# Kernel optimization log

Measured on AMD Instinct MI355X. Metric: run time of the kernel, lower is better.

## Reference

```python
import jax, jax.numpy as jnp
import numpy as np

B, S, K, D = 128, 64, 10, 256
THR = -1.5


def setup_inputs() -> dict:
    key = jax.random.key(0)
    ks = jax.random.split(key, 9)
    si = 1.0 / np.sqrt(D)  # torch GRU init: U(-1/sqrt(hidden), 1/sqrt(hidden))
    u = lambda k, shape, s: jax.random.uniform(k, shape, jnp.float32, -s, s)
    return {
        "item_embs": jax.random.normal(ks[0], (B, S, K, D), jnp.float32),
        "user_embs": jax.random.normal(ks[1], (B, S, D), jnp.float32),
        "W_ih": u(ks[2], (3 * D, 2 * D), si),
        "W_hh": u(ks[3], (3 * D, D), si),
        "b_ih": u(ks[4], (3 * D,), si),
        "b_hh": u(ks[5], (3 * D,), si),
        "w_out": u(ks[6], (D,), si),
        "b_out": u(ks[7], (), si),
        "length": jax.random.randint(ks[8], (B,), 0, S),
    }


def reference(item_embs, user_embs, W_ih, W_hh, b_ih, b_hh, w_out, b_out, length):
    N = B * S
    # x['items'] = cat([item_embs.flatten(0,1), zeros_like(...)], -1)  -> [N, K, 2D]
    items_flat = item_embs.reshape(N, K, D)
    items = jnp.concatenate([items_flat, jnp.zeros_like(items_flat)], axis=-1)
    # user hidden state: gather user_embs at (length-1, clamped), repeat over S
    idx = jnp.clip(length - 1, 0, None)  # [B]
    u0 = user_embs[jnp.arange(B), idx]   # [B, D]
    h0 = jnp.repeat(u0, S, axis=0)       # [N, D]

    def gru_cell(x, h):
        gi = x @ W_ih.T + b_ih  # [N, 3D]
        gh = h @ W_hh.T + b_hh
        i_r, i_z, i_n = jnp.split(gi, 3, axis=-1)
        h_r, h_z, h_n = jnp.split(gh, 3, axis=-1)
        r = jax.nn.sigmoid(i_r + h_r)
        z = jax.nn.sigmoid(i_z + h_z)
        n = jnp.tanh(i_n + r * h_n)
        return (1.0 - z) * n + z * h

    def step(carry, x_t):
        h, mask = carry  # mask [N,1]: readout threshold gate for the click-half of input
        x = jnp.concatenate([x_t[:, :D], x_t[:, D:] * mask], axis=-1)
        h = gru_cell(x, h)
        y = h @ w_out + b_out  # [N]
        next_mask = (jax.lax.stop_gradient(y) > THR).astype(x_t.dtype)[:, None]
        return (h, next_mask), y

    xs = jnp.swapaxes(items, 0, 1)  # [K, N, 2D]
    init = (h0, jnp.ones((N, 1), item_embs.dtype))
    _, ys = jax.lax.scan(step, init, xs)  # ys [K, N]
    y = jnp.swapaxes(ys, 0, 1)  # [N, K]
    # self.w = 1, self.b = 0 -> identity calibration
    return y.reshape(B, S, K)
```

## Files before the change

### kernel.cpp

```cpp
#include <hip/hip_runtime.h>

#define BB 128
#define SS 64
#define KK 10
#define DD 256
#define NN (BB*SS)
#define ROWS 32
#define NBLK (NN/ROWS)
#define NT 1024

typedef __attribute__((ext_vector_type(8))) short short8;
typedef __attribute__((ext_vector_type(4))) float f32x4;

#define FRAG_ELEMS (48*8*64*8)

__device__ __forceinline__ unsigned short f2bf(float f){
  union { float f; unsigned u; } v; v.f = f;
  unsigned r = (v.u + 0x7FFFu + ((v.u >> 16) & 1u)) >> 16;
  return (unsigned short)r;
}

__global__ void prep_weights(const float* __restrict__ Wih,
                             const float* __restrict__ Whh,
                             unsigned short* __restrict__ fw){
  int id = blockIdx.x * 256 + threadIdx.x;
  int arr = (id >= FRAG_ELEMS);
  int r = arr ? (id - FRAG_ELEMS) : id;
  int j  = r & 7;
  int l  = (r >> 3) & 63;
  int tk = (r >> 9) & 7;
  int tn = r >> 12;
  int c  = tn * 16 + (l & 15);
  int d  = tk * 32 + ((l >> 4) << 3) + j;
  float v = arr ? Whh[c * 256 + d] : Wih[c * 512 + d];
  fw[id] = f2bf(v);
}

__global__ __launch_bounds__(NT, 4) void gru_main(
    const float* __restrict__ item, const float* __restrict__ user,
    const float* __restrict__ b_ih, const float* __restrict__ b_hh,
    const float* __restrict__ w_out, const float* __restrict__ b_out,
    const int* __restrict__ length, const unsigned short* __restrict__ ws,
    float* __restrict__ out)
{
  __shared__ unsigned short xfrag[2][2*8*64*8];
  __shared__ unsigned short hfrag[2][2*8*64*8];
  __shared__ float yp[3][16][2][4][4];

  const int tid  = threadIdx.x;
  const int lane = tid & 63;
  const int w    = tid >> 6;
  const int col  = lane & 15;
  const int q    = lane >> 4;
  const int nb   = blockIdx.x * ROWS;
  const int b    = nb / SS;

  const short8* fw1 = (const short8*)ws;
  const short8* fwh = fw1 + (FRAG_ELEMS/8);

  const int d    = w*16 + col;
  const float br_  = b_ih[d]       + b_hh[d];
  const float bz_  = b_ih[256 + d] + b_hh[256 + d];
  const float bin_ = b_ih[512 + d];
  const float bhn_ = b_hh[512 + d];
  const float wo_  = w_out[d];

  int idx = length[b] - 1; if (idx < 0) idx = 0;
  const float u0 = user[((size_t)b*SS + idx)*DD + d];
  float h[2][4];
  #pragma unroll
  for (int mt = 0; mt < 2; ++mt)
    #pragma unroll
    for (int reg = 0; reg < 4; ++reg)
      h[mt][reg] = u0;

  const int tkk = d >> 5;
  const int slb = ((d >> 3) & 3) * 16;
  const int dj  = d & 7;
  {
    unsigned short hb = f2bf(u0);
    #pragma unroll
    for (int mt = 0; mt < 2; ++mt)
      #pragma unroll
      for (int reg = 0; reg < 4; ++reg)
        hfrag[0][((mt*8 + tkk)*64 + slb + q*4 + reg)*8 + dj] = hb;
  }

  const int xrow = tid >> 5;
  const int xo   = tid & 31;
  const int xmt  = xrow >> 4;
  const int xtk  = xo >> 2;
  const int xsl  = (xo & 3)*16 + (xrow & 15);
  {
    const float4* p = (const float4*)(item + ((size_t)(nb + xrow)*KK + 0)*DD + xo*8);
    float4 a0 = p[0], a1 = p[1];
    unsigned short t[8];
    t[0]=f2bf(a0.x); t[1]=f2bf(a0.y); t[2]=f2bf(a0.z); t[3]=f2bf(a0.w);
    t[4]=f2bf(a1.x); t[5]=f2bf(a1.y); t[6]=f2bf(a1.z); t[7]=f2bf(a1.w);
    *(short8*)&xfrag[0][((xmt*8 + xtk)*64 + xsl)*8] = *(short8*)t;
  }
  __syncthreads();

  const float bout = b_out[0];

  for (int k = 0; k < KK; ++k){
    const int cb  = k & 1;
    const int nbf = cb ^ 1;

    f32x4 acc[2][4];
    #pragma unroll
    for (int mt = 0; mt < 2; ++mt)
      #pragma unroll
      for (int kd = 0; kd < 4; ++kd){
        f32x4 z4 = {0.f, 0.f, 0.f, 0.f};
        acc[mt][kd] = z4;
      }

    #pragma unroll 2
    for (int tk = 0; tk < 8; ++tk){
      short8 ax0 = *(const short8*)&xfrag[cb][((0*8 + tk)*64 + lane)*8];
      short8 ax1 = *(const short8*)&xfrag[cb][((1*8 + tk)*64 + lane)*8];
      short8 ah0 = *(const short8*)&hfrag[cb][((0*8 + tk)*64 + lane)*8];
      short8 ah1 = *(const short8*)&hfrag[cb][((1*8 + tk)*64 + lane)*8];
      short8 w1r = fw1[((w     )*8 + tk)*64 + lane];
      short8 w1z = fw1[((16 + w)*8 + tk)*64 + lane];
      short8 w1n = fw1[((32 + w)*8 + tk)*64 + lane];
      short8 whr = fwh[((w     )*8 + tk)*64 + lane];
      short8 whz = fwh[((16 + w)*8 + tk)*64 + lane];
      short8 whn = fwh[((32 + w)*8 + tk)*64 + lane];
      acc[0][0] = __builtin_amdgcn_mfma_f32_16x16x32_bf16(ax0, w1r, acc[0][0], 0, 0, 0);
      acc[0][0] = __builtin_amdgcn_mfma_f32_16x16x32_bf16(ah0, whr, acc[0][0], 0, 0, 0);
      acc[0][1] = __builtin_amdgcn_mfma_f32_16x16x32_bf16(ax0, w1z, acc[0][1], 0, 0, 0);
      acc[0][1] = __builtin_amdgcn_mfma_f32_16x16x32_bf16(ah0, whz, acc[0][1], 0, 0, 0);
      acc[0][2] = __builtin_amdgcn_mfma_f32_16x16x32_bf16(ax0, w1n, acc[0][2], 0, 0, 0);
      acc[0][3] = __builtin_amdgcn_mfma_f32_16x16x32_bf16(ah0, whn, acc[0][3], 0, 0, 0);
      acc[1][0] = __builtin_amdgcn_mfma_f32_16x16x32_bf16(ax1, w1r, acc[1][0], 0, 0, 0);
      acc[1][0] = __builtin_amdgcn_mfma_f32_16x16x32_bf16(ah1, whr, acc[1][0], 0, 0, 0);
      acc[1][1] = __builtin_amdgcn_mfma_f32_16x16x32_bf16(ax1, w1z, acc[1][1], 0, 0, 0);
      acc[1][1] = __builtin_amdgcn_mfma_f32_16x16x32_bf16(ah1, whz, acc[1][1], 0, 0, 0);
      acc[1][2] = __builtin_amdgcn_mfma_f32_16x16x32_bf16(ax1, w1n, acc[1][2], 0, 0, 0);
      acc[1][3] = __builtin_amdgcn_mfma_f32_16x16x32_bf16(ah1, whn, acc[1][3], 0, 0, 0);
    }

    float4 xn0, xn1;
    if (k < KK-1){
      const float4* p = (const float4*)(item + ((size_t)(nb + xrow)*KK + (k+1))*DD + xo*8);
      xn0 = p[0]; xn1 = p[1];
    }

    float ypl[2][4];
    #pragma unroll
    for (int mt = 0; mt < 2; ++mt)
      #pragma unroll
      for (int reg = 0; reg < 4; ++reg){
        float rp = acc[mt][0][reg] + br_;
        float zp = acc[mt][1][reg] + bz_;
        float r  = 1.f / (1.f + __expf(-rp));
        float z  = 1.f / (1.f + __expf(-zp));
        float np = acc[mt][2][reg] + bin_ + r*(acc[mt][3][reg] + bhn_);
        np = fminf(fmaxf(np, -30.f), 30.f);
        float e  = __expf(2.f*np);
        float n  = (e - 1.f) / (e + 1.f);
        float hv = (1.f - z)*n + z*h[mt][reg];
        h[mt][reg] = hv;
        ypl[mt][reg] = hv * wo_;
      }

    #pragma unroll
    for (int mt = 0; mt < 2; ++mt)
      #pragma unroll
      for (int reg = 0; reg < 4; ++reg){
        float p = ypl[mt][reg];
        p += __shfl_xor(p, 1);
        p += __shfl_xor(p, 2);
        p += __shfl_xor(p, 4);
        p += __shfl_xor(p, 8);
        if (col == 0) yp[k % 3][w][mt][q][reg] = p;
      }

    #pragma unroll
    for (int mt = 0; mt < 2; ++mt)
      #pragma unroll
      for (int reg = 0; reg < 4; ++reg)
        hfrag[nbf][((mt*8 + tkk)*64 + slb + q*4 + reg)*8 + dj] = f2bf(h[mt][reg]);

    if (k < KK-1){
      unsigned short t[8];
      t[0]=f2bf(xn0.x); t[1]=f2bf(xn0.y); t[2]=f2bf(xn0.z); t[3]=f2bf(xn0.w);
      t[4]=f2bf(xn1.x); t[5]=f2bf(xn1.y); t[6]=f2bf(xn1.z); t[7]=f2bf(xn1.w);
      *(short8*)&xfrag[nbf][((xmt*8 + xtk)*64 + xsl)*8] = *(short8*)t;
    }

    if (k > 0 && tid < 32){
      float s = bout;
      #pragma unroll
      for (int ww = 0; ww < 16; ++ww)
        s += yp[(k-1) % 3][ww][tid >> 4][(tid >> 2) & 3][tid & 3];
      out[(size_t)(nb + tid)*KK + (k-1)] = s;
    }

    __syncthreads();
  }

  if (tid < 32){
    float s = bout;
    #pragma unroll
    for (int ww = 0; ww < 16; ++ww)
      s += yp[(KK-1) % 3][ww][tid >> 4][(tid >> 2) & 3][tid & 3];
    out[(size_t)(nb + tid)*KK + (KK-1)] = s;
  }
}

extern "C" void kernel_launch(void* const* d_in, const int* in_sizes, int n_in,
                              void* d_out, int out_size, void* d_ws, size_t ws_size,
                              hipStream_t stream) {
  const float* item   = (const float*)d_in[0];
  const float* user   = (const float*)d_in[1];
  const float* W_ih   = (const float*)d_in[2];
  const float* W_hh   = (const float*)d_in[3];
  const float* b_ih   = (const float*)d_in[4];
  const float* b_hh   = (const float*)d_in[5];
  const float* w_out  = (const float*)d_in[6];
  const float* b_out  = (const float*)d_in[7];
  const int*   length = (const int*)d_in[8];
  unsigned short* ws  = (unsigned short*)d_ws;
  float* out = (float*)d_out;

  hipLaunchKernelGGL(prep_weights, dim3((2*FRAG_ELEMS)/256), dim3(256), 0, stream,
                     W_ih, W_hh, ws);
  hipLaunchKernelGGL(gru_main, dim3(NBLK), dim3(NT), 0, stream,
                     item, user, b_ih, b_hh, w_out, b_out, length, ws, out);
}
```

Before: 230.1 us.

## Software-pipeline weight loads in registers and hoist next-step item prefetch

Adds a two-slot register double buffer for the per-warp weight fragments, so each k-tile's six global weight loads are issued two tiles ahead, wrapping across time steps. The next time step's item loads move ahead of the MFMA loop so their global latency overlaps the matrix work. The MFMA issue order is interleaved across the two row tiles to spread out accumulator dependencies, and __syncthreads is replaced by an inline-asm LDS-only wait plus barrier. The cost is higher register pressure under launch_bounds(1024,4) and a barrier that relies on the compiler tracking outstanding global loads correctly.

Measured after the change: 516.6 us. +124.5%, slower.

```diff
diff --git a/kernel.cpp b/kernel.cpp
--- a/kernel.cpp
+++ b/kernel.cpp
@@ -18,6 +18,10 @@
   union { float f; unsigned u; } v; v.f = f;
   unsigned r = (v.u + 0x7FFFu + ((v.u >> 16) & 1u)) >> 16;
   return (unsigned short)r;
+}
+
+__device__ __forceinline__ void lds_barrier(){
+  asm volatile("s_waitcnt lgkmcnt(0)\n\ts_barrier" ::: "memory");
 }
 
 __global__ void prep_weights(const float* __restrict__ Wih,
@@ -58,6 +62,13 @@
   const short8* fw1 = (const short8*)ws;
   const short8* fwh = fw1 + (FRAG_ELEMS/8);
 
+  const short8* wbase0 = fw1 + (size_t)((w     )*8)*64 + lane;
+  const short8* wbase1 = fw1 + (size_t)((16 + w)*8)*64 + lane;
+  const short8* wbase2 = fw1 + (size_t)((32 + w)*8)*64 + lane;
+  const short8* wbase3 = fwh + (size_t)((w     )*8)*64 + lane;
+  const short8* wbase4 = fwh + (size_t)((16 + w)*8)*64 + lane;
+  const short8* wbase5 = fwh + (size_t)((32 + w)*8)*64 + lane;
+
   const int d    = w*16 + col;
   const float br_  = b_ih[d]       + b_hh[d];
   const float bz_  = b_ih[256 + d] + b_hh[256 + d];
@@ -99,13 +110,31 @@
     t[4]=f2bf(a1.x); t[5]=f2bf(a1.y); t[6]=f2bf(a1.z); t[7]=f2bf(a1.w);
     *(short8*)&xfrag[0][((xmt*8 + xtk)*64 + xsl)*8] = *(short8*)t;
   }
-  __syncthreads();
+
+  short8 Wb[2][6];
+  #pragma unroll
+  for (int s = 0; s < 2; ++s){
+    Wb[s][0] = wbase0[s*64];
+    Wb[s][1] = wbase1[s*64];
+    Wb[s][2] = wbase2[s*64];
+    Wb[s][3] = wbase3[s*64];
+    Wb[s][4] = wbase4[s*64];
+    Wb[s][5] = wbase5[s*64];
+  }
+
+  lds_barrier();
 
   const float bout = b_out[0];
 
   for (int k = 0; k < KK; ++k){
     const int cb  = k & 1;
     const int nbf = cb ^ 1;
+
+    float4 xn0, xn1;
+    if (k < KK-1){
+      const float4* p = (const float4*)(item + ((size_t)(nb + xrow)*KK + (k+1))*DD + xo*8);
+      xn0 = p[0]; xn1 = p[1];
+    }
 
     f32x4 acc[2][4];
     #pragma unroll
@@ -116,36 +145,36 @@
         acc[mt][kd] = z4;
       }
 
-    #pragma unroll 2
+    #pragma unroll
     for (int tk = 0; tk < 8; ++tk){
+      const int slot = tk & 1;
+      short8 w1r = Wb[slot][0], w1z = Wb[slot][1], w1n = Wb[slot][2];
+      short8 whr = Wb[slot][3], whz = Wb[slot][4], whn = Wb[slot][5];
+      const int nx = (tk + 2) & 7;
+      Wb[slot][0] = wbase0[nx*64];
+      Wb[slot][1] = wbase1[nx*64];
+      Wb[slot][2] = wbase2[nx*64];
+      Wb[slot][3] = wbase3[nx*64];
+      Wb[slot][4] = wbase4[nx*64];
+      Wb[slot][5] = wbase5[nx*64];
+
       short8 ax0 = *(const short8*)&xfrag[cb][((0*8 + tk)*64 + lane)*8];
       short8 ax1 = *(const short8*)&xfrag[cb][((1*8 + tk)*64 + lane)*8];
       short8 ah0 = *(const short8*)&hfrag[cb][((0*8 + tk)*64 + lane)*8];
       short8 ah1 = *(const short8*)&hfrag[cb][((1*8 + tk)*64 + lane)*8];
-      short8 w1r = fw1[((w     )*8 + tk)*64 + lane];
-      short8 w1z = fw1[((16 + w)*8 + tk)*64 + lane];
-      short8 w1n = fw1[((32 + w)*8 + tk)*64 + lane];
-      short8 whr = fwh[((w     )*8 + tk)*64 + lane];
-      short8 whz = fwh[((16 + w)*8 + tk)*64 + lane];
-      short8 whn = fwh[((32 + w)*8 + tk)*64 + lane];
+
       acc[0][0] = __builtin_amdgcn_mfma_f32_16x16x32_bf16(ax0, w1r, acc[0][0], 0, 0, 0);
+      acc[1][0] = __builtin_amdgcn_mfma_f32_16x16x32_bf16(ax1, w1r, acc[1][0], 0, 0, 0);
       acc[0][0] = __builtin_amdgcn_mfma_f32_16x16x32_bf16(ah0, whr, acc[0][0], 0, 0, 0);
+      acc[1][0] = __builtin_amdgcn_mfma_f32_16x16x32_bf16(ah1, whr, acc[1][0], 0, 0, 0);
       acc[0][1] = __builtin_amdgcn_mfma_f32_16x16x32_bf16(ax0, w1z, acc[0][1], 0, 0, 0);
+      acc[1][1] = __builtin_amdgcn_mfma_f32_16x16x32_bf16(ax1, w1z, acc[1][1], 0, 0, 0);
       acc[0][1] = __builtin_amdgcn_mfma_f32_16x16x32_bf16(ah0, whz, acc[0][1], 0, 0, 0);
+      acc[1][1] = __builtin_amdgcn_mfma_f32_16x16x32_bf16(ah1, whz, acc[1][1], 0, 0, 0);
       acc[0][2] = __builtin_amdgcn_mfma_f32_16x16x32_bf16(ax0, w1n, acc[0][2], 0, 0, 0);
+      acc[1][2] = __builtin_amdgcn_mfma_f32_16x16x32_bf16(ax1, w1n, acc[1][2], 0, 0, 0);
       acc[0][3] = __builtin_amdgcn_mfma_f32_16x16x32_bf16(ah0, whn, acc[0][3], 0, 0, 0);
-      acc[1][0] = __builtin_amdgcn_mfma_f32_16x16x32_bf16(ax1, w1r, acc[1][0], 0, 0, 0);
-      acc[1][0] = __builtin_amdgcn_mfma_f32_16x16x32_bf16(ah1, whr, acc[1][0], 0, 0, 0);
-      acc[1][1] = __builtin_amdgcn_mfma_f32_16x16x32_bf16(ax1, w1z, acc[1][1], 0, 0, 0);
-      acc[1][1] = __builtin_amdgcn_mfma_f32_16x16x32_bf16(ah1, whz, acc[1][1], 0, 0, 0);
-      acc[1][2] = __builtin_amdgcn_mfma_f32_16x16x32_bf16(ax1, w1n, acc[1][2], 0, 0, 0);
       acc[1][3] = __builtin_amdgcn_mfma_f32_16x16x32_bf16(ah1, whn, acc[1][3], 0, 0, 0);
-    }
-
-    float4 xn0, xn1;
-    if (k < KK-1){
-      const float4* p = (const float4*)(item + ((size_t)(nb + xrow)*KK + (k+1))*DD + xo*8);
-      xn0 = p[0]; xn1 = p[1];
     }
 
     float ypl[2][4];
@@ -199,7 +228,7 @@
       out[(size_t)(nb + tid)*KK + (k-1)] = s;
     }
 
-    __syncthreads();
+    lds_barrier();
   }
 
   if (tid < 32){
```

## Batch input projections for two timesteps to share W_ih fragment loads

Applied to the files above, without the earlier changes.

The recurrence is processed in pairs of timesteps. The input-to-hidden MFMAs for both steps run together in one pass, so each W_ih fragment loaded from global memory feeds twice as many MFMAs. The second step's input-gate results are held in registers as packed bf16 until needed, and the hidden-to-hidden matmul is done separately per step. This cuts W_ih global/L2 traffic in half and fully unrolls the k-loops, at the cost of more register pressure and some extra rounding on the stored gate pre-activations.

After: 487.3 us. +111.7%, slower.

```diff
diff --git a/kernel.cpp b/kernel.cpp
--- a/kernel.cpp
+++ b/kernel.cpp
@@ -8,6 +8,7 @@
 #define ROWS 32
 #define NBLK (NN/ROWS)
 #define NT 1024
+#define NSUP (KK/2)
 
 typedef __attribute__((ext_vector_type(8))) short short8;
 typedef __attribute__((ext_vector_type(4))) float f32x4;
@@ -18,6 +19,15 @@
   union { float f; unsigned u; } v; v.f = f;
   unsigned r = (v.u + 0x7FFFu + ((v.u >> 16) & 1u)) >> 16;
   return (unsigned short)r;
+}
+__device__ __forceinline__ unsigned packbf2(float a, float b){
+  return (unsigned)f2bf(a) | ((unsigned)f2bf(b) << 16);
+}
+__device__ __forceinline__ float unpacklo(unsigned p){
+  union { unsigned u; float f; } v; v.u = p << 16; return v.f;
+}
+__device__ __forceinline__ float unpackhi(unsigned p){
+  union { unsigned u; float f; } v; v.u = p & 0xffff0000u; return v.f;
 }
 
 __global__ void prep_weights(const float* __restrict__ Wih,
@@ -43,7 +53,7 @@
     const int* __restrict__ length, const unsigned short* __restrict__ ws,
     float* __restrict__ out)
 {
-  __shared__ unsigned short xfrag[2][2*8*64*8];
+  __shared__ unsigned short xs[2][2][2*8*64*8];
   __shared__ unsigned short hfrag[2][2*8*64*8];
   __shared__ float yp[3][16][2][4][4];
 
@@ -91,114 +101,239 @@
   const int xmt  = xrow >> 4;
   const int xtk  = xo >> 2;
   const int xsl  = (xo & 3)*16 + (xrow & 15);
-  {
-    const float4* p = (const float4*)(item + ((size_t)(nb + xrow)*KK + 0)*DD + xo*8);
+  const int xdst = ((xmt*8 + xtk)*64 + xsl)*8;
+
+  #pragma unroll
+  for (int s = 0; s < 2; ++s){
+    const float4* p = (const float4*)(item + ((size_t)(nb + xrow)*KK + s)*DD + xo*8);
     float4 a0 = p[0], a1 = p[1];
     unsigned short t[8];
     t[0]=f2bf(a0.x); t[1]=f2bf(a0.y); t[2]=f2bf(a0.z); t[3]=f2bf(a0.w);
     t[4]=f2bf(a1.x); t[5]=f2bf(a1.y); t[6]=f2bf(a1.z); t[7]=f2bf(a1.w);
-    *(short8*)&xfrag[0][((xmt*8 + xtk)*64 + xsl)*8] = *(short8*)t;
+    *(short8*)&xs[0][s][xdst] = *(short8*)t;
   }
   __syncthreads();
 
   const float bout = b_out[0];
 
-  for (int k = 0; k < KK; ++k){
-    const int cb  = k & 1;
+  for (int j = 0; j < NSUP; ++j){
+    const int k0  = 2*j;
+    const int k1  = 2*j + 1;
+    const int cb  = j & 1;
     const int nbf = cb ^ 1;
 
-    f32x4 acc[2][4];
+    f32x4 g0[2][3];
+    f32x4 g1[2][3];
     #pragma unroll
     for (int mt = 0; mt < 2; ++mt)
       #pragma unroll
-      for (int kd = 0; kd < 4; ++kd){
-        f32x4 z4 = {0.f, 0.f, 0.f, 0.f};
-        acc[mt][kd] = z4;
-      }
-
-    #pragma unroll 2
+      for (int g = 0; g < 3; ++g){
+        f32x4 z4 = {0.f,0.f,0.f,0.f};
+        g0[mt][g] = z4; g1[mt][g] = z4;
+      }
+
+    #pragma unroll
     for (int tk = 0; tk < 8; ++tk){
-      short8 ax0 = *(const short8*)&xfrag[cb][((0*8 + tk)*64 + lane)*8];
-      short8 ax1 = *(const short8*)&xfrag[cb][((1*8 + tk)*64 + lane)*8];
-      short8 ah0 = *(const short8*)&hfrag[cb][((0*8 + tk)*64 + lane)*8];
-      short8 ah1 = *(const short8*)&hfrag[cb][((1*8 + tk)*64 + lane)*8];
       short8 w1r = fw1[((w     )*8 + tk)*64 + lane];
       short8 w1z = fw1[((16 + w)*8 + tk)*64 + lane];
       short8 w1n = fw1[((32 + w)*8 + tk)*64 + lane];
-      short8 whr = fwh[((w     )*8 + tk)*64 + lane];
-      short8 whz = fwh[((16 + w)*8 + tk)*64 + lane];
-      short8 whn = fwh[((32 + w)*8 + tk)*64 + lane];
-      acc[0][0] = __builtin_amdgcn_mfma_f32_16x16x32_bf16(ax0, w1r, acc[0][0], 0, 0, 0);
-      acc[0][0] = __builtin_amdgcn_mfma_f32_16x16x32_bf16(ah0, whr, acc[0][0], 0, 0, 0);
-      acc[0][1] = __builtin_amdgcn_mfma_f32_16x16x32_bf16(ax0, w1z, acc[0][1], 0, 0, 0);
-      acc[0][1] = __builtin_amdgcn_mfma_f32_16x16x32_bf16(ah0, whz, acc[0][1], 0, 0, 0);
-      acc[0][2] = __builtin_amdgcn_mfma_f32_16x16x32_bf16(ax0, w1n, acc[0][2], 0, 0, 0);
-      acc[0][3] = __builtin_amdgcn_mfma_f32_16x16x32_bf16(ah0, whn, acc[0][3], 0, 0, 0);
-      acc[1][0] = __builtin_amdgcn_mfma_f32_16x16x32_bf16(ax1, w1r, acc[1][0], 0, 0, 0);
-      acc[1][0] = __builtin_amdgcn_mfma_f32_16x16x32_bf16(ah1, whr, acc[1][0], 0, 0, 0);
-      acc[1][1] = __builtin_amdgcn_mfma_f32_16x16x32_bf16(ax1, w1z, acc[1][1], 0, 0, 0);
-      acc[1][1] = __builtin_amdgcn_mfma_f32_16x16x32_bf16(ah1, whz, acc[1][1], 0, 0, 0);
-      acc[1][2] = __builtin_amdgcn_mfma_f32_16x16x32_bf16(ax1, w1n, acc[1][2], 0, 0, 0);
-      acc[1][3] = __builtin_amdgcn_mfma_f32_16x16x32_bf16(ah1, whn, acc[1][3], 0, 0, 0);
+      short8 a00 = *(const short8*)&xs[cb][0][((0*8 + tk)*64 + lane)*8];
+      short8 a01 = *(const short8*)&xs[cb][0][((1*8 + tk)*64 + lane)*8];
+      short8 a10 = *(const short8*)&xs[cb][1][((0*8 + tk)*64 + lane)*8];
+      short8 a11 = *(const short8*)&xs[cb][1][((1*8 + tk)*64 + lane)*8];
+      g0[0][0] = __builtin_amdgcn_mfma_f32_16x16x32_bf16(a00, w1r, g0[0][0], 0, 0, 0);
+      g0[1][0] = __builtin_amdgcn_mfma_f32_16x16x32_bf16(a01, w1r, g0[1][0], 0, 0, 0);
+      g1[0][0] = __builtin_amdgcn_mfma_f32_16x16x32_bf16(a10, w1r, g1[0][0], 0, 0, 0);
+      g1[1][0] = __builtin_amdgcn_mfma_f32_16x16x32_bf16(a11, w1r, g1[1][0], 0, 0, 0);
+      g0[0][1] = __builtin_amdgcn_mfma_f32_16x16x32_bf16(a00, w1z, g0[0][1], 0, 0, 0);
+      g0[1][1] = __builtin_amdgcn_mfma_f32_16x16x32_bf16(a01, w1z, g0[1][1], 0, 0, 0);
+      g1[0][1] = __builtin_amdgcn_mfma_f32_16x16x32_bf16(a10, w1z, g1[0][1], 0, 0, 0);
+      g1[1][1] = __builtin_amdgcn_mfma_f32_16x16x32_bf16(a11, w1z, g1[1][1], 0, 0, 0);
+      g0[0][2] = __builtin_amdgcn_mfma_f32_16x16x32_bf16(a00, w1n, g0[0][2], 0, 0, 0);
+      g0[1][2] = __builtin_amdgcn_mfma_f32_16x16x32_bf16(a01, w1n, g0[1][2], 0, 0, 0);
+      g1[0][2] = __builtin_amdgcn_mfma_f32_16x16x32_bf16(a10, w1n, g1[0][2], 0, 0, 0);
+      g1[1][2] = __builtin_amdgcn_mfma_f32_16x16x32_bf16(a11, w1n, g1[1][2], 0, 0, 0);
     }
 
-    float4 xn0, xn1;
-    if (k < KK-1){
-      const float4* p = (const float4*)(item + ((size_t)(nb + xrow)*KK + (k+1))*DD + xo*8);
-      xn0 = p[0]; xn1 = p[1];
+    unsigned p1[2][3][2];
+    #pragma unroll
+    for (int mt = 0; mt < 2; ++mt)
+      #pragma unroll
+      for (int g = 0; g < 3; ++g){
+        p1[mt][g][0] = packbf2(g1[mt][g][0], g1[mt][g][1]);
+        p1[mt][g][1] = packbf2(g1[mt][g][2], g1[mt][g][3]);
+      }
+
+    {
+      f32x4 gh[2][3];
+      #pragma unroll
+      for (int mt = 0; mt < 2; ++mt)
+        #pragma unroll
+        for (int g = 0; g < 3; ++g){
+          f32x4 z4 = {0.f,0.f,0.f,0.f};
+          gh[mt][g] = z4;
+        }
+      #pragma unroll
+      for (int tk = 0; tk < 8; ++tk){
+        short8 whr = fwh[((w     )*8 + tk)*64 + lane];
+        short8 whz = fwh[((16 + w)*8 + tk)*64 + lane];
+        short8 whn = fwh[((32 + w)*8 + tk)*64 + lane];
+        short8 ah0 = *(const short8*)&hfrag[0][((0*8 + tk)*64 + lane)*8];
+        short8 ah1 = *(const short8*)&hfrag[0][((1*8 + tk)*64 + lane)*8];
+        gh[0][0] = __builtin_amdgcn_mfma_f32_16x16x32_bf16(ah0, whr, gh[0][0], 0, 0, 0);
+        gh[1][0] = __builtin_amdgcn_mfma_f32_16x16x32_bf16(ah1, whr, gh[1][0], 0, 0, 0);
+        gh[0][1] = __builtin_amdgcn_mfma_f32_16x16x32_bf16(ah0, whz, gh[0][1], 0, 0, 0);
+        gh[1][1] = __builtin_amdgcn_mfma_f32_16x16x32_bf16(ah1, whz, gh[1][1], 0, 0, 0);
+        gh[0][2] = __builtin_amdgcn_mfma_f32_16x16x32_bf16(ah0, whn, gh[0][2], 0, 0, 0);
+        gh[1][2] = __builtin_amdgcn_mfma_f32_16x16x32_bf16(ah1, whn, gh[1][2], 0, 0, 0);
+      }
+
+      float4 xb0, xb1;
+      if (j < NSUP-1){
+        const float4* p = (const float4*)(item + ((size_t)(nb + xrow)*KK + (k0+2))*DD + xo*8);
+        xb0 = p[0]; xb1 = p[1];
+      }
+
+      float ypl[2][4];
+      #pragma unroll
+      for (int mt = 0; mt < 2; ++mt)
+        #pragma unroll
+        for (int reg = 0; reg < 4; ++reg){
+          float rp = g0[mt][0][reg] + gh[mt][0][reg] + br_;
+          float zp = g0[mt][1][reg] + gh[mt][1][reg] + bz_;
+          float r  = 1.f / (1.f + __expf(-rp));
+          float z  = 1.f / (1.f + __expf(-zp));
+          float np = g0[mt][2][reg] + bin_ + r*(gh[mt][2][reg] + bhn_);
+          np = fminf(fmaxf(np, -30.f), 30.f);
+          float e  = __expf(2.f*np);
+          float n  = (e - 1.f) / (e + 1.f);
+          float hv = (1.f - z)*n + z*h[mt][reg];
+          h[mt][reg] = hv;
+          ypl[mt][reg] = hv * wo_;
+        }
+
+      #pragma unroll
+      for (int mt = 0; mt < 2; ++mt)
+        #pragma unroll
+        for (int reg = 0; reg < 4; ++reg){
+          float p = ypl[mt][reg];
+          p += __shfl_xor(p, 1);
+          p += __shfl_xor(p, 2);
+          p += __shfl_xor(p, 4);
+          p += __shfl_xor(p, 8);
+          if (col == 0) yp[k0 % 3][w][mt][q][reg] = p;
+        }
+
+      #pragma unroll
+      for (int mt = 0; mt < 2; ++mt)
+        #pragma unroll
+        for (int reg = 0; reg < 4; ++reg)
+          hfrag[1][((mt*8 + tkk)*64 + slb + q*4 + reg)*8 + dj] = f2bf(h[mt][reg]);
+
+      if (j < NSUP-1){
+        unsigned short t[8];
+        t[0]=f2bf(xb0.x); t[1]=f2bf(xb0.y); t[2]=f2bf(xb0.z); t[3]=f2bf(xb0.w);
+        t[4]=f2bf(xb1.x); t[5]=f2bf(xb1.y); t[6]=f2bf(xb1.z); t[7]=f2bf(xb1.w);
+        *(short8*)&xs[nbf][0][xdst] = *(short8*)t;
+      }
+
+      if (j > 0 && tid < 32){
+        float s = bout;
+        #pragma unroll
+        for (int ww = 0; ww < 16; ++ww)
+          s += yp[(k0-1) % 3][ww][tid >> 4][(tid >> 2) & 3][tid & 3];
+        out[(size_t)(nb + tid)*KK + (k0-1)] = s;
+      }
     }
-
-    float ypl[2][4];
-    #pragma unroll
-    for (int mt = 0; mt < 2; ++mt)
-      #pragma unroll
-      for (int reg = 0; reg < 4; ++reg){
-        float rp = acc[mt][0][reg] + br_;
-        float zp = acc[mt][1][reg] + bz_;
-        float r  = 1.f / (1.f + __expf(-rp));
-        float z  = 1.f / (1.f + __expf(-zp));
-        float np = acc[mt][2][reg] + bin_ + r*(acc[mt][3][reg] + bhn_);
-        np = fminf(fmaxf(np, -30.f), 30.f);
-        float e  = __expf(2.f*np);
-        float n  = (e - 1.f) / (e + 1.f);
-        float hv = (1.f - z)*n + z*h[mt][reg];
-        h[mt][reg] = hv;
-        ypl[mt][reg] = hv * wo_;
-      }
-
-    #pragma unroll
-    for (int mt = 0; mt < 2; ++mt)
-      #pragma unroll
-      for (int reg = 0; reg < 4; ++reg){
-        float p = ypl[mt][reg];
-        p += __shfl_xor(p, 1);
-        p += __shfl_xor(p, 2);
-        p += __shfl_xor(p, 4);
-        p += __shfl_xor(p, 8);
-        if (col == 0) yp[k % 3][w][mt][q][reg] = p;
-      }
-
-    #pragma unroll
-    for (int mt = 0; mt < 2; ++mt)
-      #pragma unroll
-      for (int reg = 0; reg < 4; ++reg)
-        hfrag[nbf][((mt*8 + tkk)*64 + slb + q*4 + reg)*8 + dj] = f2bf(h[mt][reg]);
-
-    if (k < KK-1){
-      unsigned short t[8];
-      t[0]=f2bf(xn0.x); t[1]=f2bf(xn0.y); t[2]=f2bf(xn0.z); t[3]=f2bf(xn0.w);
-      t[4]=f2bf(xn1.x); t[5]=f2bf(xn1.y); t[6]=f2bf(xn1.z); t[7]=f2bf(xn1.w);
-      *(short8*)&xfrag[nbf][((xmt*8 + xtk)*64 + xsl)*8] = *(short8*)t;
+    __syncthreads();
+
+    {
+      f32x4 gh[2][3];
+      #pragma unroll
+      for (int mt = 0; mt < 2; ++mt)
+        #pragma unroll
+        for (int g = 0; g < 3; ++g){
+          f32x4 z4 = {0.f,0.f,0.f,0.f};
+          gh[mt][g] = z4;
+        }
+      #pragma unroll
+      for (int tk = 0; tk < 8; ++tk){
+        short8 whr = fwh[((w     )*8 + tk)*64 + lane];
+        short8 whz = fwh[((16 + w)*8 + tk)*64 + lane];
+        short8 whn = fwh[((32 + w)*8 + tk)*64 + lane];
+        short8 ah0 = *(const short8*)&hfrag[1][((0*8 + tk)*64 + lane)*8];
+        short8 ah1 = *(const short8*)&hfrag[1][((1*8 + tk)*64 + lane)*8];
+        gh[0][0] = __builtin_amdgcn_mfma_f32_16x16x32_bf16(ah0, whr, gh[0][0], 0, 0, 0);
+        gh[1][0] = __builtin_amdgcn_mfma_f32_16x16x32_bf16(ah1, whr, gh[1][0], 0, 0, 0);
+        gh[0][1] = __builtin_amdgcn_mfma_f32_16x16x32_bf16(ah0, whz, gh[0][1], 0, 0, 0);
+        gh[1][1] = __builtin_amdgcn_mfma_f32_16x16x32_bf16(ah1, whz, gh[1][1], 0, 0, 0);
+        gh[0][2] = __builtin_amdgcn_mfma_f32_16x16x32_bf16(ah0, whn, gh[0][2], 0, 0, 0);
+        gh[1][2] = __builtin_amdgcn_mfma_f32_16x16x32_bf16(ah1, whn, gh[1][2], 0, 0, 0);
+      }
+
+      float4 xb0, xb1;
+      if (j < NSUP-1){
+        const float4* p = (const float4*)(item + ((size_t)(nb + xrow)*KK + (k1+2))*DD + xo*8);
+        xb0 = p[0]; xb1 = p[1];
+      }
+
+      float ypl[2][4];
+      #pragma unroll
+      for (int mt = 0; mt < 2; ++mt)
+        #pragma unroll
+        for (int reg = 0; reg < 4; ++reg){
+          unsigned pr = p1[mt][0][reg>>1];
+          unsigned pz = p1[mt][1][reg>>1];
+          unsigned pn = p1[mt][2][reg>>1];
+          float gir = (reg & 1) ? unpackhi(pr) : unpacklo(pr);
+          float giz = (reg & 1) ? unpackhi(pz) : unpacklo(pz);
+          float gin = (reg & 1) ? unpackhi(pn) : unpacklo(pn);
+          float rp = gir + gh[mt][0][reg] + br_;
+          float zp = giz + gh[mt][1][reg] + bz_;
+          float r  = 1.f / (1.f + __expf(-rp));
+          float z  = 1.f / (1.f + __expf(-zp));
+          float np = gin + bin_ + r*(gh[mt][2][reg] + bhn_);
+          np = fminf(fmaxf(np, -30.f), 30.f);
+          float e  = __expf(2.f*np);
+          float n  = (e - 1.f) / (e + 1.f);
+          float hv = (1.f - z)*n + z*h[mt][reg];
+          h[mt][reg] = hv;
+          ypl[mt][reg] = hv * wo_;
+        }
+
+      #pragma unroll
+      for (int mt = 0; mt < 2; ++mt)
+        #pragma unroll
+        for (int reg = 0; reg < 4; ++reg){
+          float p = ypl[mt][reg];
+          p += __shfl_xor(p, 1);
+          p += __shfl_xor(p, 2);
+          p += __shfl_xor(p, 4);
+          p += __shfl_xor(p, 8);
+          if (col == 0) yp[k1 % 3][w][mt][q][reg] = p;
+        }
+
+      #pragma unroll
+      for (int mt = 0; mt < 2; ++mt)
+        #pragma unroll
+        for (int reg = 0; reg < 4; ++reg)
+          hfrag[0][((mt*8 + tkk)*64 + slb + q*4 + reg)*8 + dj] = f2bf(h[mt][reg]);
+
+      if (j < NSUP-1){
+        unsigned short t[8];
+        t[0]=f2bf(xb0.x); t[1]=f2bf(xb0.y); t[2]=f2bf(xb0.z); t[3]=f2bf(xb0.w);
+        t[4]=f2bf(xb1.x); t[5]=f2bf(xb1.y); t[6]=f2bf(xb1.z); t[7]=f2bf(xb1.w);
+        *(short8*)&xs[nbf][1][xdst] = *(short8*)t;
+      }
+
+      if (tid < 32){
+        float s = bout;
+        #pragma unroll
+        for (int ww = 0; ww < 16; ++ww)
+          s += yp[k0 % 3][ww][tid >> 4][(tid >> 2) & 3][tid & 3];
+        out[(size_t)(nb + tid)*KK + k0] = s;
+      }
     }
-
-    if (k > 0 && tid < 32){
-      float s = bout;
-      #pragma unroll
-      for (int ww = 0; ww < 16; ++ww)
-        s += yp[(k-1) % 3][ww][tid >> 4][(tid >> 2) & 3][tid & 3];
-      out[(size_t)(nb + tid)*KK + (k-1)] = s;
-    }
-
     __syncthreads();
   }
 
```

## Split input-gate GEMM out of GRU recurrence into separate precomputed kernel

Applied to the files above, without the earlier changes.

Adds a kernel that computes the input-to-hidden gate projections for all timesteps up front, two timesteps per pass so each loaded weight fragment is reused, and stores them in bf16 in the workspace. The recurrent kernel then only does the hidden-to-hidden matmul per step and reads the precomputed gates, which shortens the serial critical path. The cost is a large extra global write and read of the gate tensor (about 250 MB), an extra launch, and bf16 rounding of the gate pre-activations. The old fused kernel is kept as a fallback when the workspace is too small. Note the original code ignores the mask on the second half of the input; it multiplies zeros, so dropping it is fine.

Result: slower. 395.0 us (+71.6%).

```diff
diff --git a/kernel.cpp b/kernel.cpp
--- a/kernel.cpp
+++ b/kernel.cpp
@@ -13,11 +13,23 @@
 typedef __attribute__((ext_vector_type(4))) float f32x4;
 
 #define FRAG_ELEMS (48*8*64*8)
+#define WS_WBYTES  (2u*FRAG_ELEMS*2u)
+#define GI_BYTES   (256ull*KK*6*1024*8)
+#define WS_NEED    ((size_t)WS_WBYTES + (size_t)GI_BYTES)
 
 __device__ __forceinline__ unsigned short f2bf(float f){
   union { float f; unsigned u; } v; v.f = f;
   unsigned r = (v.u + 0x7FFFu + ((v.u >> 16) & 1u)) >> 16;
   return (unsigned short)r;
+}
+__device__ __forceinline__ unsigned packbf2(float a, float b){
+  return (unsigned)f2bf(a) | ((unsigned)f2bf(b) << 16);
+}
+__device__ __forceinline__ float unpacklo(unsigned p){
+  union { unsigned u; float f; } v; v.u = p << 16; return v.f;
+}
+__device__ __forceinline__ float unpackhi(unsigned p){
+  union { unsigned u; float f; } v; v.u = p & 0xffff0000u; return v.f;
 }
 
 __global__ void prep_weights(const float* __restrict__ Wih,
@@ -36,7 +48,253 @@
   fw[id] = f2bf(v);
 }
 
-__global__ __launch_bounds__(NT, 4) void gru_main(
+__global__ __launch_bounds__(NT, 4) void gi_gemm(
+    const float* __restrict__ item, const unsigned short* __restrict__ ws,
+    uint2* __restrict__ gi)
+{
+  __shared__ unsigned short xs[2][2][2*8*64*8];
+
+  const int tid  = threadIdx.x;
+  const int lane = tid & 63;
+  const int w    = tid >> 6;
+  const int nb   = blockIdx.x * ROWS;
+
+  const short8* fw1 = (const short8*)ws;
+
+  const int xrow = tid >> 5;
+  const int xo   = tid & 31;
+  const int xmt  = xrow >> 4;
+  const int xtk  = xo >> 2;
+  const int xsl  = (xo & 3)*16 + (xrow & 15);
+  const int xdst = ((xmt*8 + xtk)*64 + xsl)*8;
+
+  #pragma unroll
+  for (int s = 0; s < 2; ++s){
+    const float4* p = (const float4*)(item + ((size_t)(nb + xrow)*KK + s)*DD + xo*8);
+    float4 a0 = p[0], a1 = p[1];
+    unsigned short t[8];
+    t[0]=f2bf(a0.x); t[1]=f2bf(a0.y); t[2]=f2bf(a0.z); t[3]=f2bf(a0.w);
+    t[4]=f2bf(a1.x); t[5]=f2bf(a1.y); t[6]=f2bf(a1.z); t[7]=f2bf(a1.w);
+    *(short8*)&xs[0][s][xdst] = *(short8*)t;
+  }
+  __syncthreads();
+
+  for (int j = 0; j < KK/2; ++j){
+    const int cb  = j & 1;
+    const int nbf = cb ^ 1;
+
+    f32x4 ga[2][2][3];
+    #pragma unroll
+    for (int s = 0; s < 2; ++s)
+      #pragma unroll
+      for (int mt = 0; mt < 2; ++mt)
+        #pragma unroll
+        for (int gg = 0; gg < 3; ++gg){
+          f32x4 z4 = {0.f,0.f,0.f,0.f};
+          ga[s][mt][gg] = z4;
+        }
+
+    #pragma unroll
+    for (int tk = 0; tk < 8; ++tk){
+      short8 w1r = fw1[((w     )*8 + tk)*64 + lane];
+      short8 w1z = fw1[((16 + w)*8 + tk)*64 + lane];
+      short8 w1n = fw1[((32 + w)*8 + tk)*64 + lane];
+      short8 a00 = *(const short8*)&xs[cb][0][((0*8 + tk)*64 + lane)*8];
+      short8 a01 = *(const short8*)&xs[cb][0][((1*8 + tk)*64 + lane)*8];
+      short8 a10 = *(const short8*)&xs[cb][1][((0*8 + tk)*64 + lane)*8];
+      short8 a11 = *(const short8*)&xs[cb][1][((1*8 + tk)*64 + lane)*8];
+      ga[0][0][0] = __builtin_amdgcn_mfma_f32_16x16x32_bf16(a00, w1r, ga[0][0][0], 0, 0, 0);
+      ga[0][1][0] = __builtin_amdgcn_mfma_f32_16x16x32_bf16(a01, w1r, ga[0][1][0], 0, 0, 0);
+      ga[1][0][0] = __builtin_amdgcn_mfma_f32_16x16x32_bf16(a10, w1r, ga[1][0][0], 0, 0, 0);
+      ga[1][1][0] = __builtin_amdgcn_mfma_f32_16x16x32_bf16(a11, w1r, ga[1][1][0], 0, 0, 0);
+      ga[0][0][1] = __builtin_amdgcn_mfma_f32_16x16x32_bf16(a00, w1z, ga[0][0][1], 0, 0, 0);
+      ga[0][1][1] = __builtin_amdgcn_mfma_f32_16x16x32_bf16(a01, w1z, ga[0][1][1], 0, 0, 0);
+      ga[1][0][1] = __builtin_amdgcn_mfma_f32_16x16x32_bf16(a10, w1z, ga[1][0][1], 0, 0, 0);
+      ga[1][1][1] = __builtin_amdgcn_mfma_f32_16x16x32_bf16(a11, w1z, ga[1][1][1], 0, 0, 0);
+      ga[0][0][2] = __builtin_amdgcn_mfma_f32_16x16x32_bf16(a00, w1n, ga[0][0][2], 0, 0, 0);
+      ga[0][1][2] = __builtin_amdgcn_mfma_f32_16x16x32_bf16(a01, w1n, ga[0][1][2], 0, 0, 0);
+      ga[1][0][2] = __builtin_amdgcn_mfma_f32_16x16x32_bf16(a10, w1n, ga[1][0][2], 0, 0, 0);
+      ga[1][1][2] = __builtin_amdgcn_mfma_f32_16x16x32_bf16(a11, w1n, ga[1][1][2], 0, 0, 0);
+    }
+
+    if (j < KK/2 - 1){
+      #pragma unroll
+      for (int s = 0; s < 2; ++s){
+        const float4* p = (const float4*)(item + ((size_t)(nb + xrow)*KK + (2*j + 2 + s))*DD + xo*8);
+        float4 a0 = p[0], a1 = p[1];
+        unsigned short t[8];
+        t[0]=f2bf(a0.x); t[1]=f2bf(a0.y); t[2]=f2bf(a0.z); t[3]=f2bf(a0.w);
+        t[4]=f2bf(a1.x); t[5]=f2bf(a1.y); t[6]=f2bf(a1.z); t[7]=f2bf(a1.w);
+        *(short8*)&xs[nbf][s][xdst] = *(short8*)t;
+      }
+    }
+
+    #pragma unroll
+    for (int s = 0; s < 2; ++s)
+      #pragma unroll
+      for (int mt = 0; mt < 2; ++mt)
+        #pragma unroll
+        for (int gg = 0; gg < 3; ++gg){
+          uint2 pk;
+          pk.x = packbf2(ga[s][mt][gg][0], ga[s][mt][gg][1]);
+          pk.y = packbf2(ga[s][mt][gg][2], ga[s][mt][gg][3]);
+          gi[(((size_t)blockIdx.x*KK + (2*j + s))*6 + (mt*3 + gg))*1024 + tid] = pk;
+        }
+
+    __syncthreads();
+  }
+}
+
+__global__ __launch_bounds__(NT, 4) void gru_rec(
+    const float* __restrict__ user,
+    const float* __restrict__ b_ih, const float* __restrict__ b_hh,
+    const float* __restrict__ w_out, const float* __restrict__ b_out,
+    const int* __restrict__ length, const unsigned short* __restrict__ ws,
+    const uint2* __restrict__ gi, float* __restrict__ out)
+{
+  __shared__ unsigned short hfrag[2][2*8*64*8];
+  __shared__ float yp[3][16][2][4][4];
+
+  const int tid  = threadIdx.x;
+  const int lane = tid & 63;
+  const int w    = tid >> 6;
+  const int col  = lane & 15;
+  const int q    = lane >> 4;
+  const int nb   = blockIdx.x * ROWS;
+  const int b    = nb / SS;
+
+  const short8* fwh = (const short8*)ws + (FRAG_ELEMS/8);
+
+  const int d    = w*16 + col;
+  const float br_  = b_ih[d]       + b_hh[d];
+  const float bz_  = b_ih[256 + d] + b_hh[256 + d];
+  const float bin_ = b_ih[512 + d];
+  const float bhn_ = b_hh[512 + d];
+  const float wo_  = w_out[d];
+
+  int idx = length[b] - 1; if (idx < 0) idx = 0;
+  const float u0 = user[((size_t)b*SS + idx)*DD + d];
+  float h[2][4];
+  #pragma unroll
+  for (int mt = 0; mt < 2; ++mt)
+    #pragma unroll
+    for (int reg = 0; reg < 4; ++reg)
+      h[mt][reg] = u0;
+
+  const int tkk = d >> 5;
+  const int slb = ((d >> 3) & 3) * 16;
+  const int dj  = d & 7;
+  {
+    unsigned short hb = f2bf(u0);
+    #pragma unroll
+    for (int mt = 0; mt < 2; ++mt)
+      #pragma unroll
+      for (int reg = 0; reg < 4; ++reg)
+        hfrag[0][((mt*8 + tkk)*64 + slb + q*4 + reg)*8 + dj] = hb;
+  }
+  __syncthreads();
+
+  const float bout = b_out[0];
+
+  for (int k = 0; k < KK; ++k){
+    const int cb  = k & 1;
+    const int nbf = cb ^ 1;
+
+    uint2 pg[6];
+    #pragma unroll
+    for (int c = 0; c < 6; ++c)
+      pg[c] = gi[(((size_t)blockIdx.x*KK + k)*6 + c)*1024 + tid];
+
+    f32x4 gh[2][3];
+    #pragma unroll
+    for (int mt = 0; mt < 2; ++mt)
+      #pragma unroll
+      for (int gg = 0; gg < 3; ++gg){
+        f32x4 z4 = {0.f,0.f,0.f,0.f};
+        gh[mt][gg] = z4;
+      }
+    #pragma unroll
+    for (int tk = 0; tk < 8; ++tk){
+      short8 whr = fwh[((w     )*8 + tk)*64 + lane];
+      short8 whz = fwh[((16 + w)*8 + tk)*64 + lane];
+      short8 whn = fwh[((32 + w)*8 + tk)*64 + lane];
+      short8 ah0 = *(const short8*)&hfrag[cb][((0*8 + tk)*64 + lane)*8];
+      short8 ah1 = *(const short8*)&hfrag[cb][((1*8 + tk)*64 + lane)*8];
+      gh[0][0] = __builtin_amdgcn_mfma_f32_16x16x32_bf16(ah0, whr, gh[0][0], 0, 0, 0);
+      gh[1][0] = __builtin_amdgcn_mfma_f32_16x16x32_bf16(ah1, whr, gh[1][0], 0, 0, 0);
+      gh[0][1] = __builtin_amdgcn_mfma_f32_16x16x32_bf16(ah0, whz, gh[0][1], 0, 0, 0);
+      gh[1][1] = __builtin_amdgcn_mfma_f32_16x16x32_bf16(ah1, whz, gh[1][1], 0, 0, 0);
+      gh[0][2] = __builtin_amdgcn_mfma_f32_16x16x32_bf16(ah0, whn, gh[0][2], 0, 0, 0);
+      gh[1][2] = __builtin_amdgcn_mfma_f32_16x16x32_bf16(ah1, whn, gh[1][2], 0, 0, 0);
+    }
+
+    float ypl[2][4];
+    #pragma unroll
+    for (int mt = 0; mt < 2; ++mt){
+      uint2 pr = pg[mt*3 + 0];
+      uint2 pz = pg[mt*3 + 1];
+      uint2 pn = pg[mt*3 + 2];
+      #pragma unroll
+      for (int reg = 0; reg < 4; ++reg){
+        unsigned ur = (reg < 2) ? pr.x : pr.y;
+        unsigned uz = (reg < 2) ? pz.x : pz.y;
+        unsigned un = (reg < 2) ? pn.x : pn.y;
+        float gir = (reg & 1) ? unpackhi(ur) : unpacklo(ur);
+        float giz = (reg & 1) ? unpackhi(uz) : unpacklo(uz);
+        float gin = (reg & 1) ? unpackhi(un) : unpacklo(un);
+        float rp = gir + gh[mt][0][reg] + br_;
+        float zp = giz + gh[mt][1][reg] + bz_;
+        float r  = 1.f / (1.f + __expf(-rp));
+        float z  = 1.f / (1.f + __expf(-zp));
+        float np = gin + bin_ + r*(gh[mt][2][reg] + bhn_);
+        np = fminf(fmaxf(np, -30.f), 30.f);
+        float e  = __expf(2.f*np);
+        float n  = (e - 1.f) / (e + 1.f);
+        float hv = (1.f - z)*n + z*h[mt][reg];
+        h[mt][reg] = hv;
+        ypl[mt][reg] = hv * wo_;
+      }
+    }
+
+    #pragma unroll
+    for (int mt = 0; mt < 2; ++mt)
+      #pragma unroll
+      for (int reg = 0; reg < 4; ++reg){
+        float p = ypl[mt][reg];
+        p += __shfl_xor(p, 1);
+        p += __shfl_xor(p, 2);
+        p += __shfl_xor(p, 4);
+        p += __shfl_xor(p, 8);
+        if (col == 0) yp[k % 3][w][mt][q][reg] = p;
+      }
+
+    #pragma unroll
+    for (int mt = 0; mt < 2; ++mt)
+      #pragma unroll
+      for (int reg = 0; reg < 4; ++reg)
+        hfrag[nbf][((mt*8 + tkk)*64 + slb + q*4 + reg)*8 + dj] = f2bf(h[mt][reg]);
+
+    if (k > 0 && tid < 32){
+      float s = bout;
+      #pragma unroll
+      for (int ww = 0; ww < 16; ++ww)
+        s += yp[(k-1) % 3][ww][tid >> 4][(tid >> 2) & 3][tid & 3];
+      out[(size_t)(nb + tid)*KK + (k-1)] = s;
+    }
+
+    __syncthreads();
+  }
+
+  if (tid < 32){
+    float s = bout;
+    #pragma unroll
+    for (int ww = 0; ww < 16; ++ww)
+      s += yp[(KK-1) % 3][ww][tid >> 4][(tid >> 2) & 3][tid & 3];
+    out[(size_t)(nb + tid)*KK + (KK-1)] = s;
+  }
+}
+
+__global__ __launch_bounds__(NT, 4) void gru_fb(
     const float* __restrict__ item, const float* __restrict__ user,
     const float* __restrict__ b_ih, const float* __restrict__ b_hh,
     const float* __restrict__ w_out, const float* __restrict__ b_out,
@@ -228,6 +486,14 @@
 
   hipLaunchKernelGGL(prep_weights, dim3((2*FRAG_ELEMS)/256), dim3(256), 0, stream,
                      W_ih, W_hh, ws);
-  hipLaunchKernelGGL(gru_main, dim3(NBLK), dim3(NT), 0, stream,
-                     item, user, b_ih, b_hh, w_out, b_out, length, ws, out);
-}
+
+  if (ws_size >= WS_NEED){
+    uint2* gi = (uint2*)((char*)d_ws + WS_WBYTES);
+    hipLaunchKernelGGL(gi_gemm, dim3(NBLK), dim3(NT), 0, stream, item, ws, gi);
+    hipLaunchKernelGGL(gru_rec, dim3(NBLK), dim3(NT), 0, stream,
+                       user, b_ih, b_hh, w_out, b_out, length, ws, gi, out);
+  } else {
+    hipLaunchKernelGGL(gru_fb, dim3(NBLK), dim3(NT), 0, stream,
+                       item, user, b_ih, b_hh, w_out, b_out, length, ws, out);
+  }
+}
```
